# Kernel optimization log

Hardware: AMD Instinct MI355X
Metric: run time of the kernel (lower is better)

## Reference

```python
import jax, jax.numpy as jnp
import numpy as np
import math

N_HEAD = 16

def _c(a):
    # stack real/imag -> complex64
    return jax.lax.complex(a[..., 0], a[..., 1])

def _rope_phasor(T, D, dtype=jnp.float32):
    inv_freq = 1.0 / (10000.0 ** (jnp.arange(D, dtype=dtype) / D))
    t = jnp.arange(T, dtype=dtype)
    freqs = jnp.outer(t, inv_freq)  # [T, D]
    return jax.lax.complex(jnp.cos(freqs), jnp.sin(freqs))

def setup_inputs() -> dict:
    key = jax.random.key(0)
    ks = jax.random.split(key, 9)
    B, T, C = 2, 1024, 1024
    s = 0.02
    return {
        "x":  jax.random.normal(ks[0], (B, T, C, 2), jnp.float32),
        "wq": jax.random.normal(ks[1], (C, C, 2), jnp.float32) * s,
        "bq": jax.random.normal(ks[2], (C, 2), jnp.float32) * s,
        "wk": jax.random.normal(ks[3], (C, C, 2), jnp.float32) * s,
        "bk": jax.random.normal(ks[4], (C, 2), jnp.float32) * s,
        "wv": jax.random.normal(ks[5], (C, C, 2), jnp.float32) * s,
        "bv": jax.random.normal(ks[6], (C, 2), jnp.float32) * s,
        "wo": jax.random.normal(ks[7], (C, C, 2), jnp.float32) * s,
        "bo": jax.random.normal(ks[8], (C, 2), jnp.float32) * s,
    }

def reference(x, wq, bq, wk, bk, wv, bv, wo, bo):
    B, T, C, _ = x.shape
    H = N_HEAD
    D = C // H
    xc = _c(x)
    # complex linear projections: y = x @ W^T + b
    q = xc @ _c(wq).T + _c(bq)
    k = xc @ _c(wk).T + _c(bk)
    v = xc @ _c(wv).T + _c(bv)
    # [B, T, C] -> [B, H, T, D]
    q = q.reshape(B, T, H, D).transpose(0, 2, 1, 3)
    k = k.reshape(B, T, H, D).transpose(0, 2, 1, 3)
    v = v.reshape(B, T, H, D).transpose(0, 2, 1, 3)
    # complex RoPE phasor multiply
    ph = _rope_phasor(T, D)[None, None]  # [1,1,T,D]
    q = q * ph
    k = k * ph
    # complex QK^H, scaled
    score = jnp.einsum('bhtd,bhsd->bhts', q, jnp.conj(k)) / math.sqrt(D)
    # softmax over magnitude, then real-valued complex weights
    attn = jax.nn.softmax(jnp.abs(score), axis=-1)
    attn_c = jax.lax.complex(attn, jnp.zeros_like(attn))
    out = jnp.einsum('bhts,bhsd->bhtd', attn_c, v)
    out = out.transpose(0, 2, 1, 3).reshape(B, T, C)
    out = out @ _c(wo).T + _c(bo)
    # return real/imag stacked for a real-valued harness
    return jnp.stack([out.real, out.imag], axis=-1)
```

## Files before the change

kernel.cpp:

```cpp
#include <hip/hip_runtime.h>
#include <math.h>

#define T_SEQ  1024
#define C_DIM  1024
#define NH_    16
#define H_DIM  64
#define SCL    (0.125f * 1.4426950408889634f)

typedef __bf16 bf16;
typedef __bf16 bf16x4 __attribute__((ext_vector_type(4)));
typedef __bf16 bf16x8 __attribute__((ext_vector_type(8)));
typedef float  f32x4  __attribute__((ext_vector_type(4)));

#define MFMA16(a, b, c) __builtin_amdgcn_mfma_f32_16x16x32_bf16(a, b, c, 0, 0, 0)

#define GLOAD_LDS16(g, l) __builtin_amdgcn_global_load_lds( \
    (const __attribute__((address_space(1))) void*)(g),     \
    (__attribute__((address_space(3))) void*)(l), 16, 0, 0)

__device__ __forceinline__ bf16x8 neg8(bf16x8 x) {
    union { bf16x8 v; unsigned int u[4]; } t;
    t.v = x;
    t.u[0] ^= 0x80008000u; t.u[1] ^= 0x80008000u;
    t.u[2] ^= 0x80008000u; t.u[3] ^= 0x80008000u;
    return t.v;
}

__device__ __forceinline__ bf16x8 frag_sw(const bf16* plane, int row, int chunk) {
    int c = chunk ^ (row & 7);
    return *(const bf16x8*)&plane[row * 64 + c * 8];
}
__device__ __forceinline__ bf16x8 frag_sw4(const bf16* plane, int row, int chunk) {
    int c = chunk ^ (row & 3);
    return *(const bf16x8*)&plane[row * 32 + c * 8];
}

__global__ __launch_bounds__(256)
void split_all(const float* __restrict__ x,  const float* __restrict__ wq,
               const float* __restrict__ wk, const float* __restrict__ wv,
               const float* __restrict__ wo,
               bf16* Xr, bf16* Xi, bf16* Wqr, bf16* Wqi, bf16* Wkr, bf16* Wki,
               bf16* Wvr, bf16* Wvi, bf16* Wor, bf16* Woi)
{
    int z = blockIdx.y;
    if (z > 0 && blockIdx.x >= 1024) return;
    const float* in; bf16 *pr, *pi;
    if      (z == 0) { in = x;  pr = Xr;  pi = Xi;  }
    else if (z == 1) { in = wq; pr = Wqr; pi = Wqi; }
    else if (z == 2) { in = wk; pr = Wkr; pi = Wki; }
    else if (z == 3) { in = wv; pr = Wvr; pi = Wvi; }
    else             { in = wo; pr = Wor; pi = Woi; }
    int idx = (blockIdx.x * 256 + threadIdx.x) * 4;
    float4 v0 = *(const float4*)(in + (size_t)idx * 2);
    float4 v1 = *(const float4*)(in + (size_t)idx * 2 + 4);
    bf16x4 r, im;
    r[0] = (bf16)v0.x; r[1] = (bf16)v0.z; r[2] = (bf16)v1.x; r[3] = (bf16)v1.z;
    im[0] = (bf16)v0.y; im[1] = (bf16)v0.w; im[2] = (bf16)v1.y; im[3] = (bf16)v1.w;
    *(bf16x4*)(pr + idx) = r;
    *(bf16x4*)(pi + idx) = im;
}

__global__ __launch_bounds__(256)
void rope_init(float* __restrict__ rope) {
    int idx = blockIdx.x * 256 + threadIdx.x;
    int tp = idx >> 6, d = idx & 63;
    float invf = exp2f((float)d * -0.2076205059304601f);
    float fr = (float)tp * invf;
    float sn, cs; sincosf(fr, &sn, &cs);
    *(float2*)&rope[(size_t)idx * 2] = make_float2(cs, sn);
}

template<int MODE>
__device__ __forceinline__ void cgemm128(
    const bf16* __restrict__ Ar, const bf16* __restrict__ Ai,
    const bf16* __restrict__ Br, const bf16* __restrict__ Bi,
    const float* __restrict__ bias, const float* __restrict__ rope,
    bf16* __restrict__ Yr, bf16* __restrict__ Yi, int m0, int n0)
{
    __shared__ __attribute__((aligned(16))) bf16 smem[12288];
    const int t = threadIdx.x, lane = t & 63, wave = t >> 6;
    const int wm = (wave >> 1) * 64, wn = (wave & 1) * 32;
    const int lm = lane & 15, quad = lane >> 4;
    const int lr = lane >> 2;
    const int sc4 = ((lane & 3) ^ (lr & 3)) * 8;

    f32x4 accr[4][2], acci[4][2];
#pragma unroll
    for (int i = 0; i < 4; i++)
#pragma unroll
        for (int j = 0; j < 2; j++) { accr[i][j] = (f32x4)0.f; acci[i][j] = (f32x4)0.f; }

    for (int k0 = 0; k0 < C_DIM; k0 += 32) {
#pragma unroll
        for (int j = 0; j < 6; j++) {
            int c = wave + 4 * j;
            const bf16* src; bf16* dst;
            if (c < 8)       { src = Ar + (size_t)(m0 + c * 16 + lr) * C_DIM + k0 + sc4;        dst = smem + c * 512; }
            else if (c < 16) { int cc = c - 8;  src = Ai + (size_t)(m0 + cc * 16 + lr) * C_DIM + k0 + sc4; dst = smem + 4096 + cc * 512; }
            else if (c < 20) { int cc = c - 16; src = Br + (size_t)(n0 + cc * 16 + lr) * C_DIM + k0 + sc4; dst = smem + 8192 + cc * 512; }
            else             { int cc = c - 20; src = Bi + (size_t)(n0 + cc * 16 + lr) * C_DIM + k0 + sc4; dst = smem + 10240 + cc * 512; }
            GLOAD_LDS16(src, dst);
        }
        __syncthreads();

        bf16x8 ar[4], ai_[4], br_[2], bi_[2], bn_[2];
#pragma unroll
        for (int i = 0; i < 4; i++) {
            ar[i]  = frag_sw4(smem,        wm + i * 16 + lm, quad);
            ai_[i] = frag_sw4(smem + 4096, wm + i * 16 + lm, quad);
        }
#pragma unroll
        for (int j = 0; j < 2; j++) {
            br_[j] = frag_sw4(smem + 8192,  wn + j * 16 + lm, quad);
            bi_[j] = frag_sw4(smem + 10240, wn + j * 16 + lm, quad);
            bn_[j] = neg8(bi_[j]);
        }
#pragma unroll
        for (int i = 0; i < 4; i++)
#pragma unroll
            for (int j = 0; j < 2; j++) {
                accr[i][j] = MFMA16(ar[i],  br_[j], accr[i][j]);
                accr[i][j] = MFMA16(ai_[i], bn_[j], accr[i][j]);
                acci[i][j] = MFMA16(ar[i],  bi_[j], acci[i][j]);
                acci[i][j] = MFMA16(ai_[i], br_[j], acci[i][j]);
            }
        __syncthreads();
    }

    const int h = n0 >> 6, bb = m0 >> 10, tbase = m0 & (T_SEQ - 1);

    if (MODE == 1) {
#pragma unroll
        for (int i = 0; i < 4; i++)
#pragma unroll
            for (int j = 0; j < 2; j++) {
                int d = wn + j * 16 + lm;
                float2 bv = *(const float2*)&bias[2 * (n0 + d)];
#pragma unroll
                for (int r = 0; r < 4; r++) {
                    int tpos = tbase + wm + i * 16 + quad * 4 + r;
                    float2 ph = *(const float2*)&rope[((size_t)tpos * H_DIM + d) * 2];
                    float yr = accr[i][j][r] + bv.x;
                    float yi = acci[i][j][r] + bv.y;
                    accr[i][j][r] = yr * ph.x - yi * ph.y;
                    acci[i][j][r] = yr * ph.y + yi * ph.x;
                }
            }
        bf16* dsts[2] = { Yr, Yi };
#pragma unroll
        for (int pass = 0; pass < 2; pass++) {
            __syncthreads();
#pragma unroll
            for (int i = 0; i < 4; i++)
#pragma unroll
                for (int j = 0; j < 2; j++)
#pragma unroll
                    for (int r = 0; r < 4; r++)
                        smem[(wm + i * 16 + quad * 4 + r) * 72 + wn + j * 16 + lm] =
                            (bf16)(pass ? acci[i][j][r] : accr[i][j][r]);
            __syncthreads();
            bf16* dst = dsts[pass] + ((size_t)(bb * NH_ + h) * T_SEQ + tbase) * H_DIM;
#pragma unroll
            for (int p = 0; p < 4; p++) {
                int ch = t + 256 * p;
                int row = ch >> 3, o = (ch & 7) * 8;
                *(bf16x8*)&dst[row * H_DIM + o] = *(const bf16x8*)&smem[row * 72 + o];
            }
        }
    } else {
        bf16* dsts[2] = { Yr, Yi };
#pragma unroll
        for (int pass = 0; pass < 2; pass++) {
            __syncthreads();
#pragma unroll
            for (int i = 0; i < 4; i++)
#pragma unroll
                for (int j = 0; j < 2; j++) {
                    int d = wn + j * 16 + lm;
                    float2 bv = *(const float2*)&bias[2 * (n0 + d)];
                    float bb2 = pass ? bv.y : bv.x;
                    bf16x4 pk;
#pragma unroll
                    for (int r = 0; r < 4; r++)
                        pk[r] = (bf16)((pass ? acci[i][j][r] : accr[i][j][r]) + bb2);
                    *(bf16x4*)&smem[d * 136 + wm + i * 16 + quad * 4] = pk;
                }
            __syncthreads();
            bf16* dst = dsts[pass] + ((size_t)(bb * NH_ + h) * H_DIM) * T_SEQ + tbase;
#pragma unroll
            for (int p = 0; p < 4; p++) {
                int ch = t + 256 * p;
                int row = ch >> 4, o = (ch & 15) * 8;
                *(bf16x8*)&dst[(size_t)row * T_SEQ + o] = *(const bf16x8*)&smem[row * 136 + o];
            }
        }
    }
}

__global__ __launch_bounds__(256, 3)
void qkv_gemm(const bf16* __restrict__ Xr, const bf16* __restrict__ Xi,
              const bf16* __restrict__ Wqr, const bf16* __restrict__ Wqi,
              const bf16* __restrict__ Wkr, const bf16* __restrict__ Wki,
              const bf16* __restrict__ Wvr, const bf16* __restrict__ Wvi,
              const float* __restrict__ bq, const float* __restrict__ bk,
              const float* __restrict__ bv, const float* __restrict__ rope,
              bf16* Qr, bf16* Qi, bf16* Kr, bf16* Ki, bf16* Vr, bf16* Vi)
{
    int m0 = blockIdx.y * 128, n0 = blockIdx.x * 64;
    if (blockIdx.z == 0)      cgemm128<1>(Xr, Xi, Wqr, Wqi, bq, rope, Qr, Qi, m0, n0);
    else if (blockIdx.z == 1) cgemm128<1>(Xr, Xi, Wkr, Wki, bk, rope, Kr, Ki, m0, n0);
    else                      cgemm128<2>(Xr, Xi, Wvr, Wvi, bv, nullptr, Vr, Vi, m0, n0);
}

__global__ __launch_bounds__(256, 2)
void out_gemm(const bf16* __restrict__ Ar, const bf16* __restrict__ Ai,
              const bf16* __restrict__ Br, const bf16* __restrict__ Bi,
              const float* __restrict__ bias, float* __restrict__ Y)
{
    __shared__ __attribute__((aligned(16))) bf16 sm[8192];
    const int t = threadIdx.x, lane = t & 63, wave = t >> 6;
    const int lm = lane & 15, quad = lane >> 4;
    const int lr = lane >> 2;
    const int sc4 = ((lane & 3) ^ (lr & 3)) * 8;
    const int wm = (wave >> 1) * 32, wn = (wave & 1) * 32;
    const int m0 = blockIdx.y * 64, n0 = blockIdx.x * 64;

    f32x4 accr[2][2], acci[2][2];
#pragma unroll
    for (int i = 0; i < 2; i++)
#pragma unroll
        for (int j = 0; j < 2; j++) { accr[i][j] = (f32x4)0.f; acci[i][j] = (f32x4)0.f; }

    for (int k0 = 0; k0 < C_DIM; k0 += 32) {
#pragma unroll
        for (int j = 0; j < 4; j++) {
            int c = wave + 4 * j;
            const bf16* src; bf16* dst;
            if (c < 4)       { src = Ar + (size_t)(m0 + c * 16 + lr) * C_DIM + k0 + sc4;        dst = sm + c * 512; }
            else if (c < 8)  { int cc = c - 4;  src = Ai + (size_t)(m0 + cc * 16 + lr) * C_DIM + k0 + sc4; dst = sm + 2048 + cc * 512; }
            else if (c < 12) { int cc = c - 8;  src = Br + (size_t)(n0 + cc * 16 + lr) * C_DIM + k0 + sc4; dst = sm + 4096 + cc * 512; }
            else             { int cc = c - 12; src = Bi + (size_t)(n0 + cc * 16 + lr) * C_DIM + k0 + sc4; dst = sm + 6144 + cc * 512; }
            GLOAD_LDS16(src, dst);
        }
        __syncthreads();
        bf16x8 ar[2], ai_[2], br_[2], bi_[2], bn_[2];
#pragma unroll
        for (int i = 0; i < 2; i++) {
            ar[i]  = frag_sw4(sm,        wm + i * 16 + lm, quad);
            ai_[i] = frag_sw4(sm + 2048, wm + i * 16 + lm, quad);
        }
#pragma unroll
        for (int j = 0; j < 2; j++) {
            br_[j] = frag_sw4(sm + 4096, wn + j * 16 + lm, quad);
            bi_[j] = frag_sw4(sm + 6144, wn + j * 16 + lm, quad);
            bn_[j] = neg8(bi_[j]);
        }
#pragma unroll
        for (int i = 0; i < 2; i++)
#pragma unroll
            for (int j = 0; j < 2; j++) {
                accr[i][j] = MFMA16(ar[i],  br_[j], accr[i][j]);
                accr[i][j] = MFMA16(ai_[i], bn_[j], accr[i][j]);
                acci[i][j] = MFMA16(ar[i],  bi_[j], acci[i][j]);
                acci[i][j] = MFMA16(ai_[i], br_[j], acci[i][j]);
            }
        __syncthreads();
    }
#pragma unroll
    for (int i = 0; i < 2; i++)
#pragma unroll
        for (int j = 0; j < 2; j++) {
            int n = n0 + wn + j * 16 + lm;
            float2 bv = *(const float2*)&bias[2 * n];
#pragma unroll
            for (int r = 0; r < 4; r++) {
                int m = m0 + wm + i * 16 + quad * 4 + r;
                *(float2*)&Y[((size_t)m * C_DIM + n) * 2] =
                    make_float2(accr[i][j][r] + bv.x, acci[i][j][r] + bv.y);
            }
        }
}

__global__ __launch_bounds__(512, 4)
void attn_mfma(const bf16* __restrict__ Qpr, const bf16* __restrict__ Qpi,
               const bf16* __restrict__ Kpr, const bf16* __restrict__ Kpi,
               const bf16* __restrict__ Vtr, const bf16* __restrict__ Vti,
               bf16* __restrict__ ABr, bf16* __restrict__ ABi)
{
    __shared__ __attribute__((aligned(16))) bf16 smem[24576];
    const int t = threadIdx.x, lane = t & 63, w = t >> 6;
    const int qg = w & 3, sh = w >> 2;
    const int lm = lane & 15, quad = lane >> 4;
    const int q0 = blockIdx.x * 64;
    const int h = blockIdx.y, b = blockIdx.z;
    const size_t hb = (size_t)(b * NH_ + h) * T_SEQ * H_DIM;
    const int s_lr = lane >> 3, s_c = (lane & 7) ^ s_lr;
    const int lr4 = lane >> 2, sc4 = ((lane & 3) ^ (lr4 & 3)) * 8;

    {
        const bf16* gq = (sh == 0 ? Qpr : Qpi) + hb + (size_t)q0 * H_DIM;
        bf16* lq = smem + sh * 4096;
#pragma unroll
        for (int j = 0; j < 2; j++) {
            int cc = qg * 2 + j;
            GLOAD_LDS16(gq + (cc * 8 + s_lr) * H_DIM + s_c * 8, lq + cc * 512);
        }
    }
    __syncthreads();

    bf16x8 qfr[2], qfi[2], nqfr[2];
#pragma unroll
    for (int kh = 0; kh < 2; kh++) {
        qfr[kh]  = frag_sw(smem,        qg * 16 + lm, kh * 4 + quad);
        qfi[kh]  = frag_sw(smem + 4096, qg * 16 + lm, kh * 4 + quad);
        nqfr[kh] = neg8(qfr[kh]);
    }

    bf16* Ks_r = smem + 8192 + sh * 8192;
    bf16* Ks_i = Ks_r + 2048;
    bf16* Vs_r = Ks_r + 4096;
    bf16* Vs_i = Ks_r + 6144;
    bf16* Pl   = smem;
    const int prow = sh * 64 + qg * 16 + lm;

    f32x4 Or[4], Oi[4];
#pragma unroll
    for (int nt = 0; nt < 4; nt++) { Or[nt] = (f32x4)0.f; Oi[nt] = (f32x4)0.f; }
    float mold = 0.f, lsum = 0.f;

    for (int it = 0; it < 16; it++) {
        const int s0 = it * 32 + sh * 512;
        __syncthreads();
        {
            if (qg < 2) {
                const bf16* gsrc = (qg == 0 ? Kpr : Kpi) + hb + (size_t)s0 * H_DIM;
                bf16* ldst = (qg == 0) ? Ks_r : Ks_i;
#pragma unroll
                for (int cc = 0; cc < 4; cc++)
                    GLOAD_LDS16(gsrc + (cc * 8 + s_lr) * H_DIM + s_c * 8, ldst + cc * 512);
            } else {
                const bf16* gsrc = (qg == 2 ? Vtr : Vti) + hb + s0;
                bf16* ldst = (qg == 2) ? Vs_r : Vs_i;
#pragma unroll
                for (int cc = 0; cc < 4; cc++)
                    GLOAD_LDS16(gsrc + (size_t)(cc * 16 + lr4) * T_SEQ + sc4, ldst + cc * 512);
            }
        }
        __syncthreads();

        float sc[2][4];
#pragma unroll
        for (int ct = 0; ct < 2; ct++) {
            f32x4 sre = (f32x4)0.f, sim = (f32x4)0.f;
#pragma unroll
            for (int kh = 0; kh < 2; kh++) {
                bf16x8 kr = frag_sw(Ks_r, ct * 16 + lm, kh * 4 + quad);
                bf16x8 ki = frag_sw(Ks_i, ct * 16 + lm, kh * 4 + quad);
                sre = MFMA16(kr, qfr[kh],  sre);
                sre = MFMA16(ki, qfi[kh],  sre);
                sim = MFMA16(kr, qfi[kh],  sim);
                sim = MFMA16(ki, nqfr[kh], sim);
            }
#pragma unroll
            for (int r = 0; r < 4; r++)
                sc[ct][r] = sqrtf(sre[r] * sre[r] + sim[r] * sim[r]) * SCL;
        }

        float mx = sc[0][0];
#pragma unroll
        for (int ct = 0; ct < 2; ct++)
#pragma unroll
            for (int r = 0; r < 4; r++) mx = fmaxf(mx, sc[ct][r]);
        mx = fmaxf(mx, __shfl_xor(mx, 16));
        mx = fmaxf(mx, __shfl_xor(mx, 32));
        float mnew = fmaxf(mold, mx);
        float alpha = exp2f(mold - mnew);
        float ps = 0.f;
#pragma unroll
        for (int ct = 0; ct < 2; ct++) {
            bf16x4 pk;
#pragma unroll
            for (int r = 0; r < 4; r++) {
                float p = exp2f(sc[ct][r] - mnew);
                ps += p;
                pk[r] = (bf16)p;
            }
            *(bf16x4*)&Pl[prow * 32 + ((ct * 2 + (quad >> 1)) ^ (prow & 3)) * 8
                          + (quad & 1) * 4] = pk;
        }
        ps += __shfl_xor(ps, 16);
        ps += __shfl_xor(ps, 32);
        lsum = lsum * alpha + ps;
        mold = mnew;

        float aO[4];
#pragma unroll
        for (int r = 0; r < 4; r++)
            aO[r] = __shfl(alpha, (quad << 4) + quad * 4 + r, 64);
#pragma unroll
        for (int nt = 0; nt < 4; nt++)
#pragma unroll
            for (int r = 0; r < 4; r++) { Or[nt][r] *= aO[r]; Oi[nt][r] *= aO[r]; }

        bf16x8 pf = frag_sw4(Pl, prow, quad);
#pragma unroll
        for (int nt = 0; nt < 4; nt++) {
            Or[nt] = MFMA16(pf, frag_sw4(Vs_r, nt * 16 + lm, quad), Or[nt]);
            Oi[nt] = MFMA16(pf, frag_sw4(Vs_i, nt * 16 + lm, quad), Oi[nt]);
        }
    }

    float* Of = (float*)(smem + 8192);
    float* ml = (float*)smem;
    __syncthreads();
    if (sh == 1) {
#pragma unroll
        for (int nt = 0; nt < 4; nt++)
#pragma unroll
            for (int r = 0; r < 4; r++) {
                Of[((qg * 2 + 0) * 16 + quad * 4 + r) * 64 + nt * 16 + lm] = Or[nt][r];
                Of[((qg * 2 + 1) * 16 + quad * 4 + r) * 64 + nt * 16 + lm] = Oi[nt][r];
            }
        if (quad == 0) *(float2*)&ml[(qg * 16 + lm) * 2] = make_float2(mold, lsum);
    }
    __syncthreads();
    if (sh == 0) {
        float2 m2 = *(const float2*)&ml[(qg * 16 + lm) * 2];
        float mn = fmaxf(mold, m2.x);
        float a1 = exp2f(mold - mn), a2 = exp2f(m2.x - mn);
        lsum = a1 * lsum + a2 * m2.y;
        float a1r[4], a2r[4], linv[4];
        float lv = 1.f / lsum;
#pragma unroll
        for (int r = 0; r < 4; r++) {
            int src = (quad << 4) + quad * 4 + r;
            a1r[r]  = __shfl(a1, src, 64);
            a2r[r]  = __shfl(a2, src, 64);
            linv[r] = __shfl(lv, src, 64);
        }
        size_t mbase = (size_t)(b * T_SEQ + q0 + qg * 16 + quad * 4) * C_DIM;
        int colb = h * H_DIM + lm;
#pragma unroll
        for (int nt = 0; nt < 4; nt++)
#pragma unroll
            for (int r = 0; r < 4; r++) {
                float orv = a1r[r] * Or[nt][r] +
                            a2r[r] * Of[((qg * 2 + 0) * 16 + quad * 4 + r) * 64 + nt * 16 + lm];
                float oiv = a1r[r] * Oi[nt][r] +
                            a2r[r] * Of[((qg * 2 + 1) * 16 + quad * 4 + r) * 64 + nt * 16 + lm];
                size_t o = mbase + (size_t)r * C_DIM + colb + nt * 16;
                ABr[o] = (bf16)(orv * linv[r]);
                ABi[o] = (bf16)(oiv * linv[r]);
            }
    }
}

extern "C" void kernel_launch(void* const* d_in, const int* in_sizes, int n_in,
                              void* d_out, int out_size, void* d_ws, size_t ws_size,
                              hipStream_t stream) {
    const float* x  = (const float*)d_in[0];
    const float* wq = (const float*)d_in[1];
    const float* bq = (const float*)d_in[2];
    const float* wk = (const float*)d_in[3];
    const float* bk = (const float*)d_in[4];
    const float* wv = (const float*)d_in[5];
    const float* bv = (const float*)d_in[6];
    const float* wo = (const float*)d_in[7];
    const float* bo = (const float*)d_in[8];

    float* rope = (float*)d_ws;
    bf16* w = (bf16*)(rope + 131072);
    const size_t MSZ = (size_t)2048 * 1024;
    const size_t WSZ = (size_t)1024 * 1024;
    const size_t PSZ = (size_t)2 * NH_ * T_SEQ * H_DIM;

    bf16 *Xr = w, *Xi = Xr + MSZ;
    bf16 *Wqr = Xi + MSZ,  *Wqi = Wqr + WSZ;
    bf16 *Wkr = Wqi + WSZ, *Wki = Wkr + WSZ;
    bf16 *Wvr = Wki + WSZ, *Wvi = Wvr + WSZ;
    bf16 *Wor = Wvi + WSZ, *Woi = Wor + WSZ;
    bf16 *Qr = Woi + WSZ, *Qi = Qr + PSZ;
    bf16 *Kr = Qi + PSZ,  *Ki = Kr + PSZ;
    bf16 *Vr = Ki + PSZ,  *Vi = Vr + PSZ;
    bf16 *ABr = Vi + PSZ, *ABi = ABr + MSZ;

    split_all<<<dim3(2048, 5), 256, 0, stream>>>(x, wq, wk, wv, wo,
        Xr, Xi, Wqr, Wqi, Wkr, Wki, Wvr, Wvi, Wor, Woi);
    rope_init<<<256, 256, 0, stream>>>(rope);

    qkv_gemm<<<dim3(16, 16, 3), 256, 0, stream>>>(
        Xr, Xi, Wqr, Wqi, Wkr, Wki, Wvr, Wvi, bq, bk, bv, rope,
        Qr, Qi, Kr, Ki, Vr, Vi);

    attn_mfma<<<dim3(16, 16, 2), 512, 0, stream>>>(
        Qr, Qi, Kr, Ki, Vr, Vi, ABr, ABi);

    out_gemm<<<dim3(16, 32), 256, 0, stream>>>(ABr, ABi, Wor, Woi, bo, (float*)d_out);
}
```

Before: 249.6 us.

## Double GEMM K-step to 64, merge rope init into split, pad attention P tile

The QKV and output GEMMs now stage a K-slice of 64 instead of 32 per iteration, using an 8-chunk XOR swizzle. This halves the number of barrier pairs and loop iterations but doubles LDS per block: 48 KB for qkv and 32 KB for out_gemm. out_gemm's launch bound rises to 4 blocks. The rope table computation is folded into split_all as an extra grid slice, removing one kernel launch. The attention P staging buffer switches from an XOR swizzle to a padded row stride of 40, which must fit the existing Pl allocation.

```diff
diff --git a/kernel.cpp b/kernel.cpp
--- a/kernel.cpp
+++ b/kernel.cpp
@@ -40,9 +40,20 @@
                const float* __restrict__ wk, const float* __restrict__ wv,
                const float* __restrict__ wo,
                bf16* Xr, bf16* Xi, bf16* Wqr, bf16* Wqi, bf16* Wkr, bf16* Wki,
-               bf16* Wvr, bf16* Wvi, bf16* Wor, bf16* Woi)
+               bf16* Wvr, bf16* Wvi, bf16* Wor, bf16* Woi,
+               float* __restrict__ rope)
 {
     int z = blockIdx.y;
+    if (z == 5) {
+        if (blockIdx.x >= 256) return;
+        int idx = blockIdx.x * 256 + threadIdx.x;
+        int tp = idx >> 6, d = idx & 63;
+        float invf = exp2f((float)d * -0.2076205059304601f);
+        float fr = (float)tp * invf;
+        float sn, cs; sincosf(fr, &sn, &cs);
+        *(float2*)&rope[(size_t)idx * 2] = make_float2(cs, sn);
+        return;
+    }
     if (z > 0 && blockIdx.x >= 1024) return;
     const float* in; bf16 *pr, *pi;
     if      (z == 0) { in = x;  pr = Xr;  pi = Xi;  }
@@ -60,16 +71,6 @@
     *(bf16x4*)(pi + idx) = im;
 }
 
-__global__ __launch_bounds__(256)
-void rope_init(float* __restrict__ rope) {
-    int idx = blockIdx.x * 256 + threadIdx.x;
-    int tp = idx >> 6, d = idx & 63;
-    float invf = exp2f((float)d * -0.2076205059304601f);
-    float fr = (float)tp * invf;
-    float sn, cs; sincosf(fr, &sn, &cs);
-    *(float2*)&rope[(size_t)idx * 2] = make_float2(cs, sn);
-}
-
 template<int MODE>
 __device__ __forceinline__ void cgemm128(
     const bf16* __restrict__ Ar, const bf16* __restrict__ Ai,
@@ -77,12 +78,11 @@
     const float* __restrict__ bias, const float* __restrict__ rope,
     bf16* __restrict__ Yr, bf16* __restrict__ Yi, int m0, int n0)
 {
-    __shared__ __attribute__((aligned(16))) bf16 smem[12288];
+    __shared__ __attribute__((aligned(16))) bf16 smem[24576];
     const int t = threadIdx.x, lane = t & 63, wave = t >> 6;
     const int wm = (wave >> 1) * 64, wn = (wave & 1) * 32;
     const int lm = lane & 15, quad = lane >> 4;
-    const int lr = lane >> 2;
-    const int sc4 = ((lane & 3) ^ (lr & 3)) * 8;
+    const int s_lr = lane >> 3, s_c = (lane & 7) ^ s_lr;
 
     f32x4 accr[4][2], acci[4][2];
 #pragma unroll
@@ -90,40 +90,43 @@
 #pragma unroll
         for (int j = 0; j < 2; j++) { accr[i][j] = (f32x4)0.f; acci[i][j] = (f32x4)0.f; }
 
-    for (int k0 = 0; k0 < C_DIM; k0 += 32) {
-#pragma unroll
-        for (int j = 0; j < 6; j++) {
+    for (int k0 = 0; k0 < C_DIM; k0 += 64) {
+#pragma unroll
+        for (int j = 0; j < 12; j++) {
             int c = wave + 4 * j;
             const bf16* src; bf16* dst;
-            if (c < 8)       { src = Ar + (size_t)(m0 + c * 16 + lr) * C_DIM + k0 + sc4;        dst = smem + c * 512; }
-            else if (c < 16) { int cc = c - 8;  src = Ai + (size_t)(m0 + cc * 16 + lr) * C_DIM + k0 + sc4; dst = smem + 4096 + cc * 512; }
-            else if (c < 20) { int cc = c - 16; src = Br + (size_t)(n0 + cc * 16 + lr) * C_DIM + k0 + sc4; dst = smem + 8192 + cc * 512; }
-            else             { int cc = c - 20; src = Bi + (size_t)(n0 + cc * 16 + lr) * C_DIM + k0 + sc4; dst = smem + 10240 + cc * 512; }
+            if (c < 16)      {             src = Ar + (size_t)(m0 + c * 8 + s_lr) * C_DIM + k0 + s_c * 8; dst = smem + c * 512; }
+            else if (c < 32) { int u = c - 16; src = Ai + (size_t)(m0 + u * 8 + s_lr) * C_DIM + k0 + s_c * 8; dst = smem + 8192 + u * 512; }
+            else if (c < 40) { int u = c - 32; src = Br + (size_t)(n0 + u * 8 + s_lr) * C_DIM + k0 + s_c * 8; dst = smem + 16384 + u * 512; }
+            else             { int u = c - 40; src = Bi + (size_t)(n0 + u * 8 + s_lr) * C_DIM + k0 + s_c * 8; dst = smem + 20480 + u * 512; }
             GLOAD_LDS16(src, dst);
         }
         __syncthreads();
 
-        bf16x8 ar[4], ai_[4], br_[2], bi_[2], bn_[2];
-#pragma unroll
-        for (int i = 0; i < 4; i++) {
-            ar[i]  = frag_sw4(smem,        wm + i * 16 + lm, quad);
-            ai_[i] = frag_sw4(smem + 4096, wm + i * 16 + lm, quad);
-        }
-#pragma unroll
-        for (int j = 0; j < 2; j++) {
-            br_[j] = frag_sw4(smem + 8192,  wn + j * 16 + lm, quad);
-            bi_[j] = frag_sw4(smem + 10240, wn + j * 16 + lm, quad);
-            bn_[j] = neg8(bi_[j]);
-        }
-#pragma unroll
-        for (int i = 0; i < 4; i++)
+#pragma unroll
+        for (int kh = 0; kh < 2; kh++) {
+            bf16x8 ar[4], ai_[4], br_[2], bi_[2], bn_[2];
+#pragma unroll
+            for (int i = 0; i < 4; i++) {
+                ar[i]  = frag_sw(smem,        wm + i * 16 + lm, kh * 4 + quad);
+                ai_[i] = frag_sw(smem + 8192, wm + i * 16 + lm, kh * 4 + quad);
+            }
 #pragma unroll
             for (int j = 0; j < 2; j++) {
-                accr[i][j] = MFMA16(ar[i],  br_[j], accr[i][j]);
-                accr[i][j] = MFMA16(ai_[i], bn_[j], accr[i][j]);
-                acci[i][j] = MFMA16(ar[i],  bi_[j], acci[i][j]);
-                acci[i][j] = MFMA16(ai_[i], br_[j], acci[i][j]);
-            }
+                br_[j] = frag_sw(smem + 16384, wn + j * 16 + lm, kh * 4 + quad);
+                bi_[j] = frag_sw(smem + 20480, wn + j * 16 + lm, kh * 4 + quad);
+                bn_[j] = neg8(bi_[j]);
+            }
+#pragma unroll
+            for (int i = 0; i < 4; i++)
+#pragma unroll
+                for (int j = 0; j < 2; j++) {
+                    accr[i][j] = MFMA16(ar[i],  br_[j], accr[i][j]);
+                    accr[i][j] = MFMA16(ai_[i], bn_[j], accr[i][j]);
+                    acci[i][j] = MFMA16(ar[i],  bi_[j], acci[i][j]);
+                    acci[i][j] = MFMA16(ai_[i], br_[j], acci[i][j]);
+                }
+        }
         __syncthreads();
     }
 
@@ -212,16 +215,15 @@
     else                      cgemm128<2>(Xr, Xi, Wvr, Wvi, bv, nullptr, Vr, Vi, m0, n0);
 }
 
-__global__ __launch_bounds__(256, 2)
+__global__ __launch_bounds__(256, 4)
 void out_gemm(const bf16* __restrict__ Ar, const bf16* __restrict__ Ai,
               const bf16* __restrict__ Br, const bf16* __restrict__ Bi,
               const float* __restrict__ bias, float* __restrict__ Y)
 {
-    __shared__ __attribute__((aligned(16))) bf16 sm[8192];
+    __shared__ __attribute__((aligned(16))) bf16 sm[16384];
     const int t = threadIdx.x, lane = t & 63, wave = t >> 6;
     const int lm = lane & 15, quad = lane >> 4;
-    const int lr = lane >> 2;
-    const int sc4 = ((lane & 3) ^ (lr & 3)) * 8;
+    const int s_lr = lane >> 3, s_c = (lane & 7) ^ s_lr;
     const int wm = (wave >> 1) * 32, wn = (wave & 1) * 32;
     const int m0 = blockIdx.y * 64, n0 = blockIdx.x * 64;
 
@@ -231,39 +233,42 @@
 #pragma unroll
         for (int j = 0; j < 2; j++) { accr[i][j] = (f32x4)0.f; acci[i][j] = (f32x4)0.f; }
 
-    for (int k0 = 0; k0 < C_DIM; k0 += 32) {
-#pragma unroll
-        for (int j = 0; j < 4; j++) {
+    for (int k0 = 0; k0 < C_DIM; k0 += 64) {
+#pragma unroll
+        for (int j = 0; j < 8; j++) {
             int c = wave + 4 * j;
             const bf16* src; bf16* dst;
-            if (c < 4)       { src = Ar + (size_t)(m0 + c * 16 + lr) * C_DIM + k0 + sc4;        dst = sm + c * 512; }
-            else if (c < 8)  { int cc = c - 4;  src = Ai + (size_t)(m0 + cc * 16 + lr) * C_DIM + k0 + sc4; dst = sm + 2048 + cc * 512; }
-            else if (c < 12) { int cc = c - 8;  src = Br + (size_t)(n0 + cc * 16 + lr) * C_DIM + k0 + sc4; dst = sm + 4096 + cc * 512; }
-            else             { int cc = c - 12; src = Bi + (size_t)(n0 + cc * 16 + lr) * C_DIM + k0 + sc4; dst = sm + 6144 + cc * 512; }
+            if (c < 8)       {             src = Ar + (size_t)(m0 + c * 8 + s_lr) * C_DIM + k0 + s_c * 8; dst = sm + c * 512; }
+            else if (c < 16) { int u = c - 8;  src = Ai + (size_t)(m0 + u * 8 + s_lr) * C_DIM + k0 + s_c * 8; dst = sm + 4096 + u * 512; }
+            else if (c < 24) { int u = c - 16; src = Br + (size_t)(n0 + u * 8 + s_lr) * C_DIM + k0 + s_c * 8; dst = sm + 8192 + u * 512; }
+            else             { int u = c - 24; src = Bi + (size_t)(n0 + u * 8 + s_lr) * C_DIM + k0 + s_c * 8; dst = sm + 12288 + u * 512; }
             GLOAD_LDS16(src, dst);
         }
         __syncthreads();
-        bf16x8 ar[2], ai_[2], br_[2], bi_[2], bn_[2];
-#pragma unroll
-        for (int i = 0; i < 2; i++) {
-            ar[i]  = frag_sw4(sm,        wm + i * 16 + lm, quad);
-            ai_[i] = frag_sw4(sm + 2048, wm + i * 16 + lm, quad);
-        }
-#pragma unroll
-        for (int j = 0; j < 2; j++) {
-            br_[j] = frag_sw4(sm + 4096, wn + j * 16 + lm, quad);
-            bi_[j] = frag_sw4(sm + 6144, wn + j * 16 + lm, quad);
-            bn_[j] = neg8(bi_[j]);
-        }
-#pragma unroll
-        for (int i = 0; i < 2; i++)
+#pragma unroll
+        for (int kh = 0; kh < 2; kh++) {
+            bf16x8 ar[2], ai_[2], br_[2], bi_[2], bn_[2];
+#pragma unroll
+            for (int i = 0; i < 2; i++) {
+                ar[i]  = frag_sw(sm,        wm + i * 16 + lm, kh * 4 + quad);
+                ai_[i] = frag_sw(sm + 4096, wm + i * 16 + lm, kh * 4 + quad);
+            }
 #pragma unroll
             for (int j = 0; j < 2; j++) {
-                accr[i][j] = MFMA16(ar[i],  br_[j], accr[i][j]);
-                accr[i][j] = MFMA16(ai_[i], bn_[j], accr[i][j]);
-                acci[i][j] = MFMA16(ar[i],  bi_[j], acci[i][j]);
-                acci[i][j] = MFMA16(ai_[i], br_[j], acci[i][j]);
-            }
+                br_[j] = frag_sw(sm + 8192,  wn + j * 16 + lm, kh * 4 + quad);
+                bi_[j] = frag_sw(sm + 12288, wn + j * 16 + lm, kh * 4 + quad);
+                bn_[j] = neg8(bi_[j]);
+            }
+#pragma unroll
+            for (int i = 0; i < 2; i++)
+#pragma unroll
+                for (int j = 0; j < 2; j++) {
+                    accr[i][j] = MFMA16(ar[i],  br_[j], accr[i][j]);
+                    accr[i][j] = MFMA16(ai_[i], bn_[j], accr[i][j]);
+                    acci[i][j] = MFMA16(ar[i],  bi_[j], acci[i][j]);
+                    acci[i][j] = MFMA16(ai_[i], br_[j], acci[i][j]);
+                }
+        }
         __syncthreads();
     }
 #pragma unroll
@@ -385,8 +390,7 @@
                 ps += p;
                 pk[r] = (bf16)p;
             }
-            *(bf16x4*)&Pl[prow * 32 + ((ct * 2 + (quad >> 1)) ^ (prow & 3)) * 8
-                          + (quad & 1) * 4] = pk;
+            *(bf16x4*)&Pl[prow * 40 + ct * 16 + quad * 4] = pk;
         }
         ps += __shfl_xor(ps, 16);
         ps += __shfl_xor(ps, 32);
@@ -402,7 +406,7 @@
 #pragma unroll
             for (int r = 0; r < 4; r++) { Or[nt][r] *= aO[r]; Oi[nt][r] *= aO[r]; }
 
-        bf16x8 pf = frag_sw4(Pl, prow, quad);
+        bf16x8 pf = *(const bf16x8*)&Pl[prow * 40 + quad * 8];
 #pragma unroll
         for (int nt = 0; nt < 4; nt++) {
             Or[nt] = MFMA16(pf, frag_sw4(Vs_r, nt * 16 + lm, quad), Or[nt]);
@@ -484,9 +488,8 @@
     bf16 *Vr = Ki + PSZ,  *Vi = Vr + PSZ;
     bf16 *ABr = Vi + PSZ, *ABi = ABr + MSZ;
 
-    split_all<<<dim3(2048, 5), 256, 0, stream>>>(x, wq, wk, wv, wo,
-        Xr, Xi, Wqr, Wqi, Wkr, Wki, Wvr, Wvi, Wor, Woi);
-    rope_init<<<256, 256, 0, stream>>>(rope);
+    split_all<<<dim3(2048, 6), 256, 0, stream>>>(x, wq, wk, wv, wo,
+        Xr, Xi, Wqr, Wqi, Wkr, Wki, Wvr, Wvi, Wor, Woi, rope);
 
     qkv_gemm<<<dim3(16, 16, 3), 256, 0, stream>>>(
         Xr, Xi, Wqr, Wqi, Wkr, Wki, Wvr, Wvi, bq, bk, bv, rope,
```

Result: slower. 267.1 us (+7.0%).
